# Kernel optimization log

Hardware: AMD Instinct MI355X
Metric: run time of the kernel (lower is better)

## Reference

```python
import jax, jax.numpy as jnp
import numpy as np
import math

B, S, H, NH = 1, 2048, 1024, 16  # batch, seq, hidden, heads


def setup_inputs() -> dict:
    key = jax.random.key(0)
    ks = jax.random.split(key, 12)
    inp = {
        "query": jax.random.normal(ks[0], (B, S, H), dtype=jnp.float32),
        "key": jax.random.normal(ks[1], (B, S, H), dtype=jnp.float32),
        "value": jax.random.normal(ks[2], (B, S, H), dtype=jnp.float32),
        "attention_mask": jax.random.randint(ks[3], (1, 1, S, S), 0, 2, dtype=jnp.int32),
        # torch nn.Linear params: y = x @ W.T + b, W init ~ U(-1/sqrt(H), 1/sqrt(H))
        "Wq": jax.random.uniform(ks[4], (H, H), jnp.float32, -1, 1) / math.sqrt(H),
        "bq": jax.random.uniform(ks[5], (H,), jnp.float32, -1, 1) / math.sqrt(H),
        "Wk": jax.random.uniform(ks[6], (H, H), jnp.float32, -1, 1) / math.sqrt(H),
        "bk": jax.random.uniform(ks[7], (H,), jnp.float32, -1, 1) / math.sqrt(H),
        "Wv": jax.random.uniform(ks[8], (H, H), jnp.float32, -1, 1) / math.sqrt(H),
        "bv": jax.random.uniform(ks[9], (H,), jnp.float32, -1, 1) / math.sqrt(H),
        "Wo": jax.random.uniform(ks[10], (H, H), jnp.float32, -1, 1) / math.sqrt(H),
        "bo": jax.random.uniform(ks[11], (H,), jnp.float32, -1, 1) / math.sqrt(H),
        "head": NH,
        "hidden_size": H,
    }
    return inp


def reference(query, key, value, attention_mask, Wq, bq, Wk, bk, Wv, bv, Wo, bo, head, hidden_size):
    b, s, _ = query.shape
    d_k = hidden_size // head

    def proj(x, W, bias):
        # [b, s, hidden] -> [b, head, s, d_k]
        y = x @ W.T + bias
        return y.reshape(b, s, head, d_k).transpose(0, 2, 1, 3)

    q = proj(query, Wq, bq)
    k = proj(key, Wk, bk)
    v = proj(value, Wv, bv)

    # naive full score matrix, as in the source (scale by sqrt(d_k) = last dim of q)
    scores = jnp.einsum("bhqd,bhkd->bhqk", q, k) / math.sqrt(d_k)
    # faithful quirk: masked positions are set to 0 (not -inf) before softmax
    scores = jnp.where(attention_mask == 0, jnp.zeros((), scores.dtype), scores)
    attn = jax.nn.softmax(scores, axis=-1)

    out = jnp.einsum("bhqk,bhkd->bhqd", attn, v)  # [b, head, s, d_k]
    out = out.transpose(0, 2, 1, 3).reshape(b, s, head * d_k)
    return out @ Wo.T + bo
```

## Files before the change

kernel.cpp:

```cpp
#include <hip/hip_runtime.h>
#include <hip/hip_bf16.h>


#define S_LEN 2048
#define HID   1024
#define NHEAD 16
#define DK    64

typedef unsigned short u16;
typedef __attribute__((ext_vector_type(8))) short bf16x8;
typedef __attribute__((ext_vector_type(4))) short bf16x4;
typedef __attribute__((ext_vector_type(4))) float f32x4;
typedef __attribute__((ext_vector_type(4))) unsigned u32x4;

__device__ __forceinline__ void load16_lds(const void* g, void* l) {
  __builtin_amdgcn_global_load_lds(
      (const __attribute__((address_space(1))) void*)g,
      (__attribute__((address_space(3))) void*)l, 16, 0, 0);
}

__device__ __forceinline__ short bfbits(float x) {
  __hip_bfloat16 h = __float2bfloat16(x);
  return *(short*)&h;
}
__device__ __forceinline__ bf16x8 cvt8(float4 a, float4 b) {
  bf16x8 r;
  r[0] = bfbits(a.x); r[1] = bfbits(a.y); r[2] = bfbits(a.z); r[3] = bfbits(a.w);
  r[4] = bfbits(b.x); r[5] = bfbits(b.y); r[6] = bfbits(b.z); r[7] = bfbits(b.w);
  return r;
}
__device__ __forceinline__ float bf2f(u16 u) {
  unsigned v = (unsigned)u << 16;
  return *(float*)&v;
}

__global__ __launch_bounds__(256) void cvt_pack_kernel(
    const float* __restrict__ q, const float* __restrict__ k,
    const float* __restrict__ v, const float* __restrict__ wq,
    const float* __restrict__ wk, const float* __restrict__ wv,
    const float* __restrict__ wo, const int* __restrict__ mask,
    u16* __restrict__ Xbf, u16* __restrict__ Wbf,
    unsigned int* __restrict__ bitsT) {
  const int y = blockIdx.y;
  if (y == 7) {
    if (blockIdx.x >= 512) return;
    int idx = blockIdx.x * 256 + threadIdx.x;
    int row = idx & 2047, widx = idx >> 11;
    const int4* p = (const int4*)(mask + (size_t)row * S_LEN + widx * 32);
    unsigned word = 0;
#pragma unroll
    for (int i = 0; i < 8; ++i) {
      int4 mv = p[i];
      word |= (unsigned)(mv.x != 0) << (i * 4 + 0);
      word |= (unsigned)(mv.y != 0) << (i * 4 + 1);
      word |= (unsigned)(mv.z != 0) << (i * 4 + 2);
      word |= (unsigned)(mv.w != 0) << (i * 4 + 3);
    }
    bitsT[(size_t)widx * S_LEN + row] = word;
    return;
  }
  size_t i = ((size_t)blockIdx.x * 256 + threadIdx.x) * 8;
  const float* src;
  u16* dst;
  size_t n;
  if (y < 3) {
    src = y == 0 ? q : (y == 1 ? k : v);
    dst = Xbf + (size_t)y * (S_LEN * HID);
    n = (size_t)S_LEN * HID;
  } else {
    int w = y - 3;
    src = w == 0 ? wq : (w == 1 ? wk : (w == 2 ? wv : wo));
    dst = Wbf + (size_t)w * (HID * HID);
    n = (size_t)HID * HID;
  }
  if (i >= n) return;
  float4 a = *(const float4*)(src + i);
  float4 b = *(const float4*)(src + i + 4);
  *(bf16x8*)(dst + i) = cvt8(a, b);
}

__global__ __launch_bounds__(256, 3) void gemm_qkv(
    const u16* __restrict__ Xbf, const u16* __restrict__ Wbf,
    const float* __restrict__ bq, const float* __restrict__ bk,
    const float* __restrict__ bv, u16* __restrict__ Qb,
    u16* __restrict__ Kb, u16* __restrict__ Vt) {
  constexpr int Mm = 2048, Kk = 1024, NIT = 16;
  const int tid = threadIdx.x, lane = tid & 63, wave = tid >> 6;
  const int q4 = lane >> 4, c16 = lane & 15;
  const int bx = blockIdx.x;
  const int xcd = bx & 7, s = bx >> 3;
  const int mBase = (s & 15) * 128;
  const int nG = xcd * 6 + (s >> 4);
  const int nBase = nG * 64;
  const int z = nBase >> 10;
  const u16* A = Xbf + (size_t)z * (S_LEN * HID);
  const float* bias = z == 0 ? bq : (z == 1 ? bk : bv);
  const float oscale = (z == 0) ? 0.125f * 1.44269504088896f : 1.0f;

  const int wr = wave >> 1, wc = wave & 1;

  __shared__ __align__(16) u16 As[2][2][128 * 32];
  __shared__ __align__(16) u16 Bs[2][2][64 * 32];

  f32x4 acc[4][2] = {};
  const int srow = lane >> 2;
  const int sx8 = ((lane & 3) ^ ((srow >> 1) & 3)) * 8;
  const int rx8 = (q4 ^ ((c16 >> 1) & 3)) * 8;

  auto issue = [&](int it, int buf) {
#pragma unroll
    for (int j = 0; j < 4; ++j) {
      int u = wave * 4 + j, h = u >> 3, grp = u & 7;
      load16_lds(A + (size_t)(mBase + grp * 16 + srow) * Kk + it * 64 +
                     h * 32 + sx8,
                 &As[buf][h][grp * 512]);
    }
#pragma unroll
    for (int j = 0; j < 2; ++j) {
      int u = wave * 2 + j, h = u >> 2, grp = u & 3;
      load16_lds(Wbf + (size_t)(nBase + grp * 16 + srow) * Kk + it * 64 +
                     h * 32 + sx8,
                 &Bs[buf][h][grp * 512]);
    }
  };

  issue(0, 0);
  __syncthreads();

  for (int it = 0; it < NIT; ++it) {
    const int buf = it & 1, nbuf = buf ^ 1;
    if (it + 1 < NIT) issue(it + 1, nbuf);
#pragma unroll
    for (int kk = 0; kk < 2; ++kk) {
      bf16x8 af[4], bfr[2];
#pragma unroll
      for (int t = 0; t < 4; ++t)
        af[t] = *(const bf16x8*)&As[buf][kk][(wr * 64 + t * 16 + c16) * 32 + rx8];
#pragma unroll
      for (int t = 0; t < 2; ++t)
        bfr[t] = *(const bf16x8*)&Bs[buf][kk][(wc * 32 + t * 16 + c16) * 32 + rx8];
#pragma unroll
      for (int mt = 0; mt < 4; ++mt)
#pragma unroll
        for (int nt = 0; nt < 2; ++nt)
          acc[mt][nt] = __builtin_amdgcn_mfma_f32_16x16x32_bf16(
              af[mt], bfr[nt], acc[mt][nt], 0, 0, 0);
    }
    __syncthreads();
  }

#pragma unroll
  for (int nt = 0; nt < 2; ++nt) {
    int colg = nBase + wc * 32 + nt * 16 + c16;
    int col = colg & 1023;
    float bv2 = bias[col];
#pragma unroll
    for (int mt = 0; mt < 4; ++mt) {
#pragma unroll
      for (int r = 0; r < 4; ++r) {
        int row = mBase + wr * 64 + mt * 16 + q4 * 4 + r;
        float v = (acc[mt][nt][r] + bv2) * oscale;
        if (z == 2) {
          int vv = row & 31;
          int rowp = (row & ~31) | (((vv & 15) << 1) | (vv >> 4));
          ((__hip_bfloat16*)Vt)[(size_t)col * Mm + rowp] = __float2bfloat16(v);
        } else {
          u16* C = z == 0 ? Qb : Kb;
          ((__hip_bfloat16*)C)[(size_t)row * 1024 + col] = __float2bfloat16(v);
        }
      }
    }
  }
}

__global__ __launch_bounds__(512, 4) void attn_kernel(
    const u16* __restrict__ Qb, const u16* __restrict__ Kb,
    const u16* __restrict__ Vt, const unsigned* __restrict__ mbT,
    u16* __restrict__ partOA, u16* __restrict__ partO3,
    float* __restrict__ partL) {
  constexpr int NITA = 8;
  const int lin = blockIdx.x + 8 * (blockIdx.y + 16 * blockIdx.z);
  const int work = ((lin & 7) << 6) | (lin >> 3);
  const int qt = work & 7, h = (work >> 3) & 15, zz = work >> 7;
  const int tid = threadIdx.x, lane = tid & 63, wave = tid >> 6;
  const int q4 = lane >> 4, c16 = lane & 15;

  __shared__ __align__(16) u16 Ks[2][2][64 * 32];
  __shared__ __align__(16) u16 Vs[2][2][64 * 32];
  __shared__ __align__(16) u16 Ps[8][32 * 72];

  const int q0 = qt * 256 + wave * 32;

  bf16x8 qf[2][2];
#pragma unroll
  for (int m = 0; m < 2; ++m)
#pragma unroll
    for (int kk = 0; kk < 2; ++kk)
      qf[m][kk] = *(const bf16x8*)(Qb + (size_t)(q0 + m * 16 + c16) * HID +
                                   h * DK + kk * 32 + q4 * 8);

  f32x4 o[2][4] = {};
  float l_lane[2][4] = {{}, {}};
  const unsigned mlo = 1u << c16, mhi = mlo << 16;

  const int srow = lane >> 2;
  const int sx8 = ((lane & 3) ^ ((srow >> 1) & 3)) * 8;
  const int rx8 = (q4 ^ ((c16 >> 1) & 3)) * 8;
  const int kvbase = zz * (S_LEN / 4);

  auto issueKV = [&](int it, int buf) {
    const int kv0 = kvbase + it * 64;
#pragma unroll
    for (int j = 0; j < 2; ++j) {
      int i = wave * 2 + j;
      if (i < 8) {
        int half = i >> 2, grp = i & 3;
        load16_lds(Kb + (size_t)(kv0 + grp * 16 + srow) * HID + h * DK +
                       half * 32 + sx8,
                   &Ks[buf][half][grp * 512]);
      } else {
        int ii = i - 8;
        int half = ii >> 2, grp = ii & 3;
        load16_lds(Vt + (size_t)(h * DK + grp * 16 + srow) * S_LEN + kv0 +
                       half * 32 + sx8,
                   &Vs[buf][half][grp * 512]);
      }
    }
  };

  issueKV(0, 0);
  __syncthreads();

  u16* pw = &Ps[wave][0];

  for (int it = 0; it < NITA; ++it) {
    const int buf = it & 1, nbuf = buf ^ 1;
    if (it + 1 < NITA) issueKV(it + 1, nbuf);

    const unsigned* mr = mbT + (size_t)(zz * 16 + it * 2) * S_LEN + q0 + q4 * 4;

#pragma unroll
    for (int ntp = 0; ntp < 2; ++ntp) {
      u32x4 mw0 = *(const u32x4*)(mr + (size_t)ntp * S_LEN);
      u32x4 mw1 = *(const u32x4*)(mr + (size_t)ntp * S_LEN + 16);
      f32x4 sv[2][2];
      __builtin_amdgcn_s_setprio(1);
#pragma unroll
      for (int ntb = 0; ntb < 2; ++ntb) {
        const int nt = ntp * 2 + ntb;
        const int rsw = (nt * 16 + c16) * 32 + rx8;
        bf16x8 kf0 = *(const bf16x8*)&Ks[buf][0][rsw];
        bf16x8 kf1 = *(const bf16x8*)&Ks[buf][1][rsw];
#pragma unroll
        for (int m = 0; m < 2; ++m) {
          f32x4 a = {};
          a = __builtin_amdgcn_mfma_f32_16x16x32_bf16(qf[m][0], kf0, a, 0, 0, 0);
          a = __builtin_amdgcn_mfma_f32_16x16x32_bf16(qf[m][1], kf1, a, 0, 0, 0);
          sv[m][ntb] = a;
        }
      }
      __builtin_amdgcn_s_setprio(0);
#pragma unroll
      for (int m = 0; m < 2; ++m) {
        const u32x4 mw = m ? mw1 : mw0;
#pragma unroll
        for (int r = 0; r < 4; ++r) {
          unsigned word = mw[r];
          float s0 = (word & mlo) ? sv[m][0][r] : 0.0f;
          float s1 = (word & mhi) ? sv[m][1][r] : 0.0f;
          float p0, p1;
          asm("v_exp_f32 %0, %1" : "=v"(p0) : "v"(s0));
          asm("v_exp_f32 %0, %1" : "=v"(p1) : "v"(s1));
          l_lane[m][r] += p0 + p1;
          unsigned pk;
          asm("v_cvt_pk_bf16_f32 %0, %1, %2" : "=v"(pk) : "v"(p0), "v"(p1));
          *(unsigned*)&pw[(m * 16 + q4 * 4 + r) * 72 + ntp * 32 + c16 * 2] = pk;
        }
      }
    }

    asm volatile("s_waitcnt lgkmcnt(0)" ::: "memory");

    __builtin_amdgcn_s_setprio(1);
#pragma unroll
    for (int kk = 0; kk < 2; ++kk) {
      bf16x8 pa0 = *(const bf16x8*)&pw[(c16) * 72 + kk * 32 + q4 * 8];
      bf16x8 pa1 = *(const bf16x8*)&pw[(16 + c16) * 72 + kk * 32 + q4 * 8];
#pragma unroll
      for (int nt = 0; nt < 4; ++nt) {
        const int rsw = (nt * 16 + c16) * 32 + rx8;
        bf16x8 vb = *(const bf16x8*)&Vs[buf][kk][rsw];
        o[0][nt] = __builtin_amdgcn_mfma_f32_16x16x32_bf16(pa0, vb, o[0][nt], 0, 0, 0);
        o[1][nt] = __builtin_amdgcn_mfma_f32_16x16x32_bf16(pa1, vb, o[1][nt], 0, 0, 0);
      }
    }
    __builtin_amdgcn_s_setprio(0);
    __syncthreads();
  }

  u16* pO = (zz < 3) ? (partOA + (size_t)zz * (S_LEN * HID)) : partO3;
#pragma unroll
  for (int m = 0; m < 2; ++m)
#pragma unroll
    for (int r = 0; r < 4; ++r) {
      float s = l_lane[m][r];
#pragma unroll
      for (int d = 1; d < 16; d <<= 1) s += __shfl_xor(s, d);
      int row = q0 + m * 16 + q4 * 4 + r;
#pragma unroll
      for (int nt = 0; nt < 4; ++nt)
        ((__hip_bfloat16*)pO)[(size_t)row * HID + h * DK + nt * 16 + c16] =
            __float2bfloat16(o[m][nt][r]);
      if (c16 == 0)
        partL[((size_t)zz * NHEAD + h) * S_LEN + row] = s;
    }
}

__global__ __launch_bounds__(256) void gemm_out(
    const u16* __restrict__ pOA, const u16* __restrict__ pO3,
    const float* __restrict__ partL, const u16* __restrict__ Wo,
    const float* __restrict__ bo, float* __restrict__ out) {
  constexpr int Nn = 1024, Kk = 1024, NIT = 16;
  constexpr size_t M2 = (size_t)S_LEN * HID;
  const int tid = threadIdx.x, lane = tid & 63, wave = tid >> 6;
  const int q4 = lane >> 4, c16 = lane & 15;
  const int bx = blockIdx.x;
  const int xcd = bx & 7, s = bx >> 3;
  const int mBase = (xcd * 8 + (s & 7)) * 32;
  const int nBase = (s >> 3) * 128;
  const int wn = wave * 32;

  __shared__ __align__(16) u16 As[2][2][32 * 32];
  __shared__ __align__(16) u16 Bs[2][2][128 * 32];
  __shared__ float linv[32][16];

  f32x4 acc[2][2] = {};
  const int srow = lane >> 2;
  const int sx8 = ((lane & 3) ^ ((srow >> 1) & 3)) * 8;
  const int rx8 = (q4 ^ ((c16 >> 1) & 3)) * 8;

  const int arow = tid >> 3, acu = tid & 7;
  const int ahalf = acu >> 2;
  const int aoff = arow * 32 + ((acu & 3) ^ ((arow >> 1) & 3)) * 8;

  auto issueB = [&](int it, int buf) {
#pragma unroll
    for (int j = 0; j < 4; ++j) {
      int u = wave * 4 + j, h = u >> 3, grp = u & 7;
      load16_lds(Wo + (size_t)(nBase + grp * 16 + srow) * Kk + it * 64 +
                     h * 32 + sx8,
                 &Bs[buf][h][grp * 512]);
    }
  };

  bf16x8 avA[4], avB[4];
  auto aloadTo = [&](bf16x8* dst, int it) {
    const u16* p = pOA + (size_t)(mBase + arow) * Kk + it * 64 + acu * 8;
    dst[0] = *(const bf16x8*)p;
    dst[1] = *(const bf16x8*)(p + M2);
    dst[2] = *(const bf16x8*)(p + 2 * M2);
    dst[3] = *(const bf16x8*)(pO3 + (size_t)(mBase + arow) * Kk + it * 64 + acu * 8);
  };
  auto awriteFrom = [&](const bf16x8* src, int it, int buf) {
    float inv = linv[arow][it];
    bf16x8 r;
#pragma unroll
    for (int j = 0; j < 8; ++j) {
      float v = (bf2f((u16)src[0][j]) + bf2f((u16)src[1][j]) +
                 bf2f((u16)src[2][j]) + bf2f((u16)src[3][j])) * inv;
      r[j] = bfbits(v);
    }
    *(bf16x8*)&As[buf][ahalf][aoff] = r;
  };

#pragma unroll
  for (int e = 0; e < 2; ++e) {
    int idx = tid * 2 + e, row = idx >> 4, hh = idx & 15;
    float l = 0.0f;
#pragma unroll
    for (int z = 0; z < 4; ++z)
      l += partL[(size_t)(z * NHEAD + hh) * S_LEN + mBase + row];
    linv[row][hh] = 1.0f / l;
  }
  aloadTo(avA, 0);
  issueB(0, 0);
  __syncthreads();
  awriteFrom(avA, 0, 0);
  aloadTo(avB, 1);
  __syncthreads();

  for (int it = 0; it < NIT; ++it) {
    const int buf = it & 1, nbuf = buf ^ 1;
    if (it + 1 < NIT) issueB(it + 1, nbuf);
    if (it + 2 < NIT) aloadTo((it & 1) ? avB : avA, it + 2);
#pragma unroll
    for (int kk = 0; kk < 2; ++kk) {
      bf16x8 af[2], bfr[2];
#pragma unroll
      for (int t = 0; t < 2; ++t)
        af[t] = *(const bf16x8*)&As[buf][kk][(t * 16 + c16) * 32 + rx8];
#pragma unroll
      for (int t = 0; t < 2; ++t)
        bfr[t] = *(const bf16x8*)&Bs[buf][kk][(wn + t * 16 + c16) * 32 + rx8];
#pragma unroll
      for (int mt = 0; mt < 2; ++mt)
#pragma unroll
        for (int nt = 0; nt < 2; ++nt)
          acc[mt][nt] = __builtin_amdgcn_mfma_f32_16x16x32_bf16(
              af[mt], bfr[nt], acc[mt][nt], 0, 0, 0);
    }
    if (it + 1 < NIT) awriteFrom((it & 1) ? avA : avB, it + 1, nbuf);
    __syncthreads();
  }

#pragma unroll
  for (int nt = 0; nt < 2; ++nt) {
    int col = nBase + wn + nt * 16 + c16;
    float bv = bo[col];
#pragma unroll
    for (int mt = 0; mt < 2; ++mt)
#pragma unroll
      for (int r = 0; r < 4; ++r) {
        int row = mBase + mt * 16 + q4 * 4 + r;
        out[(size_t)row * Nn + col] = acc[mt][nt][r] + bv;
      }
  }
}

extern "C" void kernel_launch(void* const* d_in, const int* in_sizes, int n_in,
                              void* d_out, int out_size, void* d_ws, size_t ws_size,
                              hipStream_t stream) {
  const float* q    = (const float*)d_in[0];
  const float* k    = (const float*)d_in[1];
  const float* v    = (const float*)d_in[2];
  const int*   mask = (const int*)d_in[3];
  const float* Wq = (const float*)d_in[4];
  const float* bq = (const float*)d_in[5];
  const float* Wk = (const float*)d_in[6];
  const float* bk = (const float*)d_in[7];
  const float* Wv = (const float*)d_in[8];
  const float* bv = (const float*)d_in[9];
  const float* Wo = (const float*)d_in[10];
  const float* bo = (const float*)d_in[11];

  const size_t M2 = (size_t)S_LEN * HID;
  const size_t W1 = (size_t)HID * HID;
  const size_t need = (4 * W1 + 3 * M2 + 3 * M2) * 2 +
                      (size_t)S_LEN * 64 * 4 + 2 * NHEAD * S_LEN * 4;
  if (ws_size < need) return;

  u16* Wbf = (u16*)d_ws;
  u16* Xbf = Wbf + 4 * W1;
  u16* Qb = Xbf + 3 * M2;
  u16* Kb = Qb + M2;
  u16* Vt = Kb + M2;
  unsigned* mbits = (unsigned*)(Vt + M2);
  u16* partOA = Xbf;
  u16* partO3 = Wbf;
  float* partL = (float*)(Wbf + 2 * W1);

  hipLaunchKernelGGL(cvt_pack_kernel, dim3(1024, 8), dim3(256), 0, stream,
                     q, k, v, Wq, Wk, Wv, Wo, mask, Xbf, Wbf, mbits);

  hipLaunchKernelGGL(gemm_qkv, dim3(768), dim3(256), 0, stream,
                     Xbf, Wbf, bq, bk, bv, Qb, Kb, Vt);

  hipLaunchKernelGGL(attn_kernel, dim3(S_LEN / 256, NHEAD, 4), dim3(512), 0,
                     stream, Qb, Kb, Vt, mbits, partOA, partO3, partL);

  hipLaunchKernelGGL(gemm_out, dim3(512), dim3(256), 0, stream,
                     partOA, partO3, partL, Wbf + 3 * W1, bo, (float*)d_out);
}
```

Measured before the change: 201.7 us.

## Keep softmax probabilities in registers by transposing score MFMA and permuting V layout

The QK^T MFMA now takes K as the A operand, so each lane holds scores for one query row across keys. The exponentiated probabilities can then be packed directly into the bf16 A-fragment for the PV MFMA, which removes the per-wave LDS staging buffer, its stores and loads, and the lgkmcnt wait. To make this work, the V transpose permutation in the QKV GEMM epilogue changes and the mask bits are stored row-major rather than transposed. The QKV GEMM block-to-tile mapping across XCDs is also remapped for cache locality. The risk is that the register-level permutation must exactly match the MFMA operand layouts, or the output is wrong.

```diff
diff --git a/kernel.cpp b/kernel.cpp
--- a/kernel.cpp
+++ b/kernel.cpp
@@ -11,6 +11,7 @@
 typedef __attribute__((ext_vector_type(8))) short bf16x8;
 typedef __attribute__((ext_vector_type(4))) short bf16x4;
 typedef __attribute__((ext_vector_type(4))) float f32x4;
+typedef __attribute__((ext_vector_type(2))) unsigned u32x2;
 typedef __attribute__((ext_vector_type(4))) unsigned u32x4;
 
 __device__ __forceinline__ void load16_lds(const void* g, void* l) {
@@ -40,13 +41,12 @@
     const float* __restrict__ wk, const float* __restrict__ wv,
     const float* __restrict__ wo, const int* __restrict__ mask,
     u16* __restrict__ Xbf, u16* __restrict__ Wbf,
-    unsigned int* __restrict__ bitsT) {
+    unsigned int* __restrict__ bits) {
   const int y = blockIdx.y;
   if (y == 7) {
     if (blockIdx.x >= 512) return;
     int idx = blockIdx.x * 256 + threadIdx.x;
-    int row = idx & 2047, widx = idx >> 11;
-    const int4* p = (const int4*)(mask + (size_t)row * S_LEN + widx * 32);
+    const int4* p = (const int4*)(mask + (size_t)idx * 32);
     unsigned word = 0;
 #pragma unroll
     for (int i = 0; i < 8; ++i) {
@@ -56,7 +56,7 @@
       word |= (unsigned)(mv.z != 0) << (i * 4 + 2);
       word |= (unsigned)(mv.w != 0) << (i * 4 + 3);
     }
-    bitsT[(size_t)widx * S_LEN + row] = word;
+    bits[idx] = word;
     return;
   }
   size_t i = ((size_t)blockIdx.x * 256 + threadIdx.x) * 8;
@@ -89,8 +89,9 @@
   const int q4 = lane >> 4, c16 = lane & 15;
   const int bx = blockIdx.x;
   const int xcd = bx & 7, s = bx >> 3;
-  const int mBase = (s & 15) * 128;
-  const int nG = xcd * 6 + (s >> 4);
+  const int mh = s / 24;
+  const int mBase = ((xcd >> 1) * 4 + mh) * 128;
+  const int nG = (xcd & 1) * 24 + (s - mh * 24);
   const int nBase = nG * 64;
   const int z = nBase >> 10;
   const u16* A = Xbf + (size_t)z * (S_LEN * HID);
@@ -162,7 +163,8 @@
         float v = (acc[mt][nt][r] + bv2) * oscale;
         if (z == 2) {
           int vv = row & 31;
-          int rowp = (row & ~31) | (((vv & 15) << 1) | (vv >> 4));
+          int rowp = (row & ~31) | (((vv & 15) >> 2) << 3) |
+                     (((vv >> 4) & 1) << 2) | (vv & 3);
           ((__hip_bfloat16*)Vt)[(size_t)col * Mm + rowp] = __float2bfloat16(v);
         } else {
           u16* C = z == 0 ? Qb : Kb;
@@ -175,7 +177,7 @@
 
 __global__ __launch_bounds__(512, 4) void attn_kernel(
     const u16* __restrict__ Qb, const u16* __restrict__ Kb,
-    const u16* __restrict__ Vt, const unsigned* __restrict__ mbT,
+    const u16* __restrict__ Vt, const unsigned* __restrict__ mb,
     u16* __restrict__ partOA, u16* __restrict__ partO3,
     float* __restrict__ partL) {
   constexpr int NITA = 8;
@@ -187,7 +189,6 @@
 
   __shared__ __align__(16) u16 Ks[2][2][64 * 32];
   __shared__ __align__(16) u16 Vs[2][2][64 * 32];
-  __shared__ __align__(16) u16 Ps[8][32 * 72];
 
   const int q0 = qt * 256 + wave * 32;
 
@@ -200,8 +201,7 @@
                                    h * DK + kk * 32 + q4 * 8);
 
   f32x4 o[2][4] = {};
-  float l_lane[2][4] = {{}, {}};
-  const unsigned mlo = 1u << c16, mhi = mlo << 16;
+  float l_lane[2] = {0.0f, 0.0f};
 
   const int srow = lane >> 2;
   const int sx8 = ((lane & 3) ^ ((srow >> 1) & 3)) * 8;
@@ -231,89 +231,91 @@
   issueKV(0, 0);
   __syncthreads();
 
-  u16* pw = &Ps[wave][0];
-
   for (int it = 0; it < NITA; ++it) {
     const int buf = it & 1, nbuf = buf ^ 1;
     if (it + 1 < NITA) issueKV(it + 1, nbuf);
 
-    const unsigned* mr = mbT + (size_t)(zz * 16 + it * 2) * S_LEN + q0 + q4 * 4;
-
-#pragma unroll
-    for (int ntp = 0; ntp < 2; ++ntp) {
-      u32x4 mw0 = *(const u32x4*)(mr + (size_t)ntp * S_LEN);
-      u32x4 mw1 = *(const u32x4*)(mr + (size_t)ntp * S_LEN + 16);
+    u32x2 mw[2];
+#pragma unroll
+    for (int m = 0; m < 2; ++m)
+      mw[m] = *(const u32x2*)(mb + (size_t)(q0 + m * 16 + c16) * 64 +
+                              (kvbase >> 5) + it * 2);
+
+#pragma unroll
+    for (int kk = 0; kk < 2; ++kk) {
       f32x4 sv[2][2];
       __builtin_amdgcn_s_setprio(1);
 #pragma unroll
       for (int ntb = 0; ntb < 2; ++ntb) {
-        const int nt = ntp * 2 + ntb;
+        const int nt = kk * 2 + ntb;
         const int rsw = (nt * 16 + c16) * 32 + rx8;
         bf16x8 kf0 = *(const bf16x8*)&Ks[buf][0][rsw];
         bf16x8 kf1 = *(const bf16x8*)&Ks[buf][1][rsw];
 #pragma unroll
         for (int m = 0; m < 2; ++m) {
           f32x4 a = {};
-          a = __builtin_amdgcn_mfma_f32_16x16x32_bf16(qf[m][0], kf0, a, 0, 0, 0);
-          a = __builtin_amdgcn_mfma_f32_16x16x32_bf16(qf[m][1], kf1, a, 0, 0, 0);
+          a = __builtin_amdgcn_mfma_f32_16x16x32_bf16(kf0, qf[m][0], a, 0, 0, 0);
+          a = __builtin_amdgcn_mfma_f32_16x16x32_bf16(kf1, qf[m][1], a, 0, 0, 0);
           sv[m][ntb] = a;
         }
       }
       __builtin_amdgcn_s_setprio(0);
+
+      bf16x8 pa[2];
 #pragma unroll
       for (int m = 0; m < 2; ++m) {
-        const u32x4 mw = m ? mw1 : mw0;
-#pragma unroll
-        for (int r = 0; r < 4; ++r) {
-          unsigned word = mw[r];
-          float s0 = (word & mlo) ? sv[m][0][r] : 0.0f;
-          float s1 = (word & mhi) ? sv[m][1][r] : 0.0f;
-          float p0, p1;
-          asm("v_exp_f32 %0, %1" : "=v"(p0) : "v"(s0));
-          asm("v_exp_f32 %0, %1" : "=v"(p1) : "v"(s1));
-          l_lane[m][r] += p0 + p1;
-          unsigned pk;
-          asm("v_cvt_pk_bf16_f32 %0, %1, %2" : "=v"(pk) : "v"(p0), "v"(p1));
-          *(unsigned*)&pw[(m * 16 + q4 * 4 + r) * 72 + ntp * 32 + c16 * 2] = pk;
-        }
-      }
-    }
-
-    asm volatile("s_waitcnt lgkmcnt(0)" ::: "memory");
-
-    __builtin_amdgcn_s_setprio(1);
-#pragma unroll
-    for (int kk = 0; kk < 2; ++kk) {
-      bf16x8 pa0 = *(const bf16x8*)&pw[(c16) * 72 + kk * 32 + q4 * 8];
-      bf16x8 pa1 = *(const bf16x8*)&pw[(16 + c16) * 72 + kk * 32 + q4 * 8];
-#pragma unroll
-      for (int nt = 0; nt < 4; ++nt) {
-        const int rsw = (nt * 16 + c16) * 32 + rx8;
+        const unsigned word = kk ? mw[m][1] : mw[m][0];
+        float p[8];
+#pragma unroll
+        for (int ntb = 0; ntb < 2; ++ntb)
+#pragma unroll
+          for (int r = 0; r < 4; ++r) {
+            const int bit = ntb * 16 + q4 * 4 + r;
+            float s = ((word >> bit) & 1u) ? sv[m][ntb][r] : 0.0f;
+            float e;
+            asm("v_exp_f32 %0, %1" : "=v"(e) : "v"(s));
+            l_lane[m] += e;
+            p[ntb * 4 + r] = e;
+          }
+        u32x4 pk;
+#pragma unroll
+        for (int j = 0; j < 4; ++j)
+          asm("v_cvt_pk_bf16_f32 %0, %1, %2"
+              : "=v"(pk[j]) : "v"(p[2 * j]), "v"(p[2 * j + 1]));
+        pa[m] = *(bf16x8*)&pk;
+      }
+
+      __builtin_amdgcn_s_setprio(1);
+#pragma unroll
+      for (int ntv = 0; ntv < 4; ++ntv) {
+        const int rsw = (ntv * 16 + c16) * 32 + rx8;
         bf16x8 vb = *(const bf16x8*)&Vs[buf][kk][rsw];
-        o[0][nt] = __builtin_amdgcn_mfma_f32_16x16x32_bf16(pa0, vb, o[0][nt], 0, 0, 0);
-        o[1][nt] = __builtin_amdgcn_mfma_f32_16x16x32_bf16(pa1, vb, o[1][nt], 0, 0, 0);
-      }
-    }
-    __builtin_amdgcn_s_setprio(0);
+        o[0][ntv] = __builtin_amdgcn_mfma_f32_16x16x32_bf16(pa[0], vb, o[0][ntv], 0, 0, 0);
+        o[1][ntv] = __builtin_amdgcn_mfma_f32_16x16x32_bf16(pa[1], vb, o[1][ntv], 0, 0, 0);
+      }
+      __builtin_amdgcn_s_setprio(0);
+    }
     __syncthreads();
   }
 
   u16* pO = (zz < 3) ? (partOA + (size_t)zz * (S_LEN * HID)) : partO3;
 #pragma unroll
-  for (int m = 0; m < 2; ++m)
+  for (int m = 0; m < 2; ++m) {
+    float s = l_lane[m];
+    s += __shfl_xor(s, 16);
+    s += __shfl_xor(s, 32);
+    int qrow = q0 + m * 16 + c16;
+    if (q4 == 0)
+      partL[((size_t)zz * NHEAD + h) * S_LEN + qrow] = s;
 #pragma unroll
     for (int r = 0; r < 4; ++r) {
-      float s = l_lane[m][r];
-#pragma unroll
-      for (int d = 1; d < 16; d <<= 1) s += __shfl_xor(s, d);
       int row = q0 + m * 16 + q4 * 4 + r;
 #pragma unroll
       for (int nt = 0; nt < 4; ++nt)
         ((__hip_bfloat16*)pO)[(size_t)row * HID + h * DK + nt * 16 + c16] =
             __float2bfloat16(o[m][nt][r]);
-      if (c16 == 0)
-        partL[((size_t)zz * NHEAD + h) * S_LEN + row] = s;
-    }
+    }
+  }
 }
 
 __global__ __launch_bounds__(256) void gemm_out(
```

Result: faster. 195.2 us (-3.2%).
